# Kernel tuning notes

Hardware: AMD Instinct MI355X
Metric: run time of the kernel (lower is better)

## Reference

```python
import jax, jax.numpy as jnp
import numpy as np


def _gcn_conv(x, W, b, src, dst, n_nodes):
    """PyG-style GCNConv: XW, symmetric deg^-1/2 normalization over edges
    (with self-loops already included in src/dst), scatter-add to targets, + bias."""
    xw = x @ W  # [N, F_out]
    ones = jnp.ones(src.shape[0], dtype=xw.dtype)
    deg = jax.ops.segment_sum(ones, dst, num_segments=n_nodes)  # in-degree incl. self-loops
    dinv = jnp.where(deg > 0, jax.lax.rsqrt(jnp.maximum(deg, 1.0)), 0.0)
    norm = dinv[src] * dinv[dst]                        # [E]
    msgs = xw[src] * norm[:, None]                      # [E, F_out] gather + scale
    out = jax.ops.segment_sum(msgs, dst, num_segments=n_nodes)  # scatter-add
    return out + b


def setup_inputs() -> dict:
    key = jax.random.key(0)
    k1, k2, k3, k4 = jax.random.split(key, 4)
    N, E = 100000, 1600000
    IN, HID, OUT = 128, 64, 64
    x = jax.random.normal(k1, (N, IN), dtype=jnp.float32)
    edge_index = jax.random.randint(k2, (2, E), 0, N, dtype=jnp.int64)
    W1 = jax.random.normal(k3, (IN, HID), dtype=jnp.float32) * (1.0 / np.sqrt(IN))
    b1 = jnp.zeros((HID,), dtype=jnp.float32)
    W2 = jax.random.normal(k4, (HID, OUT), dtype=jnp.float32) * (1.0 / np.sqrt(HID))
    b2 = jnp.zeros((OUT,), dtype=jnp.float32)
    return {"x": x, "edge_index": edge_index, "W1": W1, "b1": b1, "W2": W2, "b2": b2}


def reference(x, edge_index, W1, b1, W2, b2):
    n_nodes = x.shape[0]
    # add self-loops (PyG GCNConv default add_self_loops=True)
    loops = jnp.arange(n_nodes, dtype=edge_index.dtype)
    src = jnp.concatenate([edge_index[0], loops])
    dst = jnp.concatenate([edge_index[1], loops])
    h = _gcn_conv(x, W1, b1, src, dst, n_nodes)
    h = jax.nn.relu(h)
    z = _gcn_conv(h, W2, b2, src, dst, n_nodes)
    return z
```

## Files before the change

kernel.cpp:

```cpp
#include <hip/hip_runtime.h>

#define IN_F 128
#define HID_F 64
#define BKT_SHIFT 9
#define BKT_SIZE 512
#define CHUNK 4096

typedef unsigned short ushort_t;
typedef __attribute__((ext_vector_type(8))) short bf16x8;
typedef __attribute__((ext_vector_type(8))) unsigned short u16x8;
typedef __attribute__((ext_vector_type(4))) float f32x4;

__device__ inline ushort_t f2bf(float f) {
    unsigned u = __float_as_uint(f);
    u += 0x7FFFu + ((u >> 16) & 1u);
    return (ushort_t)(u >> 16);
}
__device__ inline float bf2f(ushort_t u) {
    return __uint_as_float((unsigned)u << 16);
}


__global__ __launch_bounds__(256) void k_hist_pack(const int* __restrict__ dst,
        int* __restrict__ ghist, int E, int nbE,
        const float* __restrict__ W1, const float* __restrict__ W2,
        ushort_t* __restrict__ Bp1, ushort_t* __restrict__ Bp2) {
    int tid = threadIdx.x;
    if ((int)blockIdx.x >= nbE) {
        int id = ((int)blockIdx.x - nbE) * 256 + tid;
        int iw = (id < 8192) ? id : id - 8192;
        int j = iw & 7, lane = (iw >> 3) & 63, t = (iw >> 9) & 3, s = iw >> 11;
        int k = s * 32 + ((lane >> 4) << 3) + j;
        int n = t * 16 + (lane & 15);
        if (id < 8192)        Bp1[iw] = f2bf(W1[k * 64 + n]);
        else if (id < 12288)  Bp2[iw] = f2bf(W2[k * 64 + n]);
        return;
    }
    __shared__ int hist[256];
    hist[tid] = 0;
    __syncthreads();
    int e0 = blockIdx.x * CHUNK, e1 = min(e0 + CHUNK, E);
    for (int e = e0 + tid; e < e1; e += 256)
        atomicAdd(&hist[dst[e] >> BKT_SHIFT], 1);
    __syncthreads();
    ghist[blockIdx.x * 256 + tid] = hist[tid];
}

__global__ __launch_bounds__(256) void k_colscan(int* __restrict__ ghist,
        int* __restrict__ gcount, int nb) {
    __shared__ int s[256];
    int t = threadIdx.x;
    int b = blockIdx.x;
    int j0 = 2 * t, j1 = 2 * t + 1;
    int v0 = (j0 < nb) ? ghist[j0 * 256 + b] : 0;
    int v1 = (j1 < nb) ? ghist[j1 * 256 + b] : 0;
    int p = v0 + v1;
    s[t] = p;
    __syncthreads();
    for (int off = 1; off < 256; off <<= 1) {
        int v = (t >= off) ? s[t - off] : 0;
        __syncthreads();
        s[t] += v;
        __syncthreads();
    }
    int excl = s[t] - p;
    if (j0 < nb) ghist[j0 * 256 + b] = excl;
    if (j1 < nb) ghist[j1 * 256 + b] = excl + v0;
    if (t == 255) gcount[b] = s[255];
}

__global__ __launch_bounds__(256) void k_scatter(const int* __restrict__ src,
        const int* __restrict__ dst, const int* __restrict__ ghist,
        const int* __restrict__ gcount, unsigned* __restrict__ gbin, int E) {
    __shared__ int cur[256];
    __shared__ int s[256];
    int tid = threadIdx.x;
    int gc = gcount[tid];
    s[tid] = gc;
    __syncthreads();
    for (int off = 1; off < 256; off <<= 1) {
        int v = (tid >= off) ? s[tid - off] : 0;
        __syncthreads();
        s[tid] += v;
        __syncthreads();
    }
    cur[tid] = ghist[blockIdx.x * 256 + tid] + (s[tid] - gc);
    __syncthreads();
    int e0 = blockIdx.x * CHUNK, e1 = min(e0 + CHUNK, E);
    for (int e = e0 + tid; e < e1; e += 256) {
        int d = dst[e];
        int b = d >> BKT_SHIFT;
        int p = atomicAdd(&cur[b], 1);
        gbin[p] = ((unsigned)(d & (BKT_SIZE - 1)) << 23) | (unsigned)src[e];
    }
}

__global__ __launch_bounds__(256) void k_fill2(const unsigned* __restrict__ gbin,
        const int* __restrict__ gcount, int* __restrict__ rowptr,
        float* __restrict__ dinv, int* __restrict__ col, int N, int E) {
    __shared__ int cnt[BKT_SIZE];
    __shared__ int pos[BKT_SIZE];
    __shared__ int s[256];
    int tid = threadIdx.x;
    int b = blockIdx.x;
    int gc = gcount[tid];
    s[tid] = gc;
    __syncthreads();
    for (int off = 1; off < 256; off <<= 1) {
        int v = (tid >= off) ? s[tid - off] : 0;
        __syncthreads();
        s[tid] += v;
        __syncthreads();
    }
    int e0 = (b > 0) ? s[b - 1] : 0;
    int e1 = s[b];
    if (b == 0 && tid == 0) rowptr[N] = E;
    __syncthreads();
    cnt[tid] = 0; cnt[tid + 256] = 0;
    __syncthreads();
    for (int e = e0 + tid; e < e1; e += 256)
        atomicAdd(&cnt[gbin[e] >> 23], 1);
    __syncthreads();
    int c0 = cnt[2 * tid], c1 = cnt[2 * tid + 1];
    int p2 = c0 + c1;
    s[tid] = p2;
    __syncthreads();
    for (int off = 1; off < 256; off <<= 1) {
        int v = (tid >= off) ? s[tid - off] : 0;
        __syncthreads();
        s[tid] += v;
        __syncthreads();
    }
    int excl = s[tid] - p2;
    pos[2 * tid] = excl;
    pos[2 * tid + 1] = excl + c0;
    __syncthreads();
    int n0 = b << BKT_SHIFT;
    #pragma unroll
    for (int i = tid; i < BKT_SIZE; i += 256) {
        int n = n0 + i;
        if (n < N) {
            rowptr[n] = e0 + pos[i];
            dinv[n] = rsqrtf((float)cnt[i] + 1.0f);
        }
    }
    __syncthreads();
    for (int t = 0; t < 8; ++t) {
        for (int e = e0 + tid; e < e1; e += 256) {
            unsigned v = gbin[e];
            if (((v >> 14) & 7u) == (unsigned)t) {
                int p = atomicAdd(&pos[v >> 23], 1);
                col[e0 + p] = (int)(v & 0x7FFFFFu);
            }
        }
        __syncthreads();
    }
}

template<int K, typename AT>
__global__ __launch_bounds__(256) void k_gemm_mfma(const AT* __restrict__ A,
        const ushort_t* __restrict__ Bp, const float* __restrict__ dinv,
        ushort_t* __restrict__ out, int N) {
    int wave = threadIdx.x >> 6, lane = threadIdx.x & 63;
    int m = lane & 15, q = lane >> 4;
    int row0 = blockIdx.x * 64 + wave * 16;
    int arow = row0 + m;
    int arowc = (arow < N) ? arow : (N - 1);
    f32x4 acc[4] = {};
    #pragma unroll
    for (int s = 0; s < K / 32; ++s) {
        bf16x8 af;
        if constexpr (sizeof(AT) == 4) {
            const float* ap = (const float*)A + (size_t)arowc * K + s * 32 + q * 8;
            float4 x0 = *(const float4*)ap;
            float4 x1 = *(const float4*)(ap + 4);
            af[0] = (short)f2bf(x0.x); af[1] = (short)f2bf(x0.y);
            af[2] = (short)f2bf(x0.z); af[3] = (short)f2bf(x0.w);
            af[4] = (short)f2bf(x1.x); af[5] = (short)f2bf(x1.y);
            af[6] = (short)f2bf(x1.z); af[7] = (short)f2bf(x1.w);
        } else {
            af = *(const bf16x8*)((const ushort_t*)A + (size_t)arowc * K + s * 32 + q * 8);
        }
        #pragma unroll
        for (int t = 0; t < 4; ++t) {
            bf16x8 bf = *(const bf16x8*)(Bp + (size_t)((s * 4 + t) * 64 + lane) * 8);
            acc[t] = __builtin_amdgcn_mfma_f32_16x16x32_bf16(af, bf, acc[t], 0, 0, 0);
        }
    }
    int orow0 = row0 + q * 4;
    float4 d4 = *(const float4*)(dinv + orow0);
    #pragma unroll
    for (int r = 0; r < 4; ++r) {
        int row = orow0 + r;
        if (row < N) {
            float dn = (r == 0) ? d4.x : (r == 1) ? d4.y : (r == 2) ? d4.z : d4.w;
            #pragma unroll
            for (int t = 0; t < 4; ++t)
                out[(size_t)row * 64 + t * 16 + m] = f2bf(acc[t][r] * dn);
        }
    }
}

__global__ __launch_bounds__(256) void k_agg_gemm(const ushort_t* __restrict__ xws,
        const int* __restrict__ rowptr, const int* __restrict__ col,
        const float* __restrict__ dinv, const float* __restrict__ bias,
        const ushort_t* __restrict__ Bp2, ushort_t* __restrict__ out2, int N) {
    __shared__ ushort_t hl[32][72];
    int tid = threadIdx.x;
    int nl = tid >> 3;
    int i = tid & 7;
    int n0 = blockIdx.x * 32;
    int n = n0 + nl;
    u16x8 hz = {};
    if (n < N) {
        int beg = rowptr[n], end = rowptr[n + 1];
        float dn = dinv[n];
        const ushort_t* base = xws + i * 8;
        u16x8 sv = *(const u16x8*)(base + (size_t)n * 64);
        float a[8];
        #pragma unroll
        for (int k = 0; k < 8; ++k) a[k] = bf2f(sv[k]);
        int e = beg;
        for (; e + 8 <= end; e += 8) {
            int c[8];
            #pragma unroll
            for (int j = 0; j < 8; ++j) c[j] = col[e + j];
            u16x8 v[8];
            #pragma unroll
            for (int j = 0; j < 8; ++j) v[j] = *(const u16x8*)(base + (size_t)c[j] * 64);
            #pragma unroll
            for (int j = 0; j < 8; ++j)
                #pragma unroll
                for (int k = 0; k < 8; ++k) a[k] += bf2f(v[j][k]);
        }
        if (e + 4 <= end) {
            int c[4];
            #pragma unroll
            for (int j = 0; j < 4; ++j) c[j] = col[e + j];
            u16x8 v[4];
            #pragma unroll
            for (int j = 0; j < 4; ++j) v[j] = *(const u16x8*)(base + (size_t)c[j] * 64);
            #pragma unroll
            for (int j = 0; j < 4; ++j)
                #pragma unroll
                for (int k = 0; k < 8; ++k) a[k] += bf2f(v[j][k]);
            e += 4;
        }
        for (; e < end; ++e) {
            u16x8 v = *(const u16x8*)(base + (size_t)col[e] * 64);
            #pragma unroll
            for (int k = 0; k < 8; ++k) a[k] += bf2f(v[k]);
        }
        float4 b0 = *(const float4*)(bias + i * 8);
        float4 b1 = *(const float4*)(bias + i * 8 + 4);
        float r[8];
        r[0] = dn * a[0] + b0.x; r[1] = dn * a[1] + b0.y;
        r[2] = dn * a[2] + b0.z; r[3] = dn * a[3] + b0.w;
        r[4] = dn * a[4] + b1.x; r[5] = dn * a[5] + b1.y;
        r[6] = dn * a[6] + b1.z; r[7] = dn * a[7] + b1.w;
        #pragma unroll
        for (int k = 0; k < 8; ++k) hz[k] = f2bf(fmaxf(r[k], 0.f));
    }
    *(u16x8*)&hl[nl][i * 8] = hz;
    __syncthreads();
    int w = tid >> 6, lane = tid & 63;
    int m = lane & 15, q = lane >> 4;
    int mt = w & 1;
    int nt0 = (w >> 1) << 1;
    f32x4 acc[2] = {};
    #pragma unroll
    for (int s = 0; s < 2; ++s) {
        bf16x8 af = *(const bf16x8*)&hl[mt * 16 + m][s * 32 + q * 8];
        #pragma unroll
        for (int tt = 0; tt < 2; ++tt) {
            bf16x8 bf = *(const bf16x8*)(Bp2 + (size_t)((s * 4 + nt0 + tt) * 64 + lane) * 8);
            acc[tt] = __builtin_amdgcn_mfma_f32_16x16x32_bf16(af, bf, acc[tt], 0, 0, 0);
        }
    }
    int orow0 = n0 + mt * 16 + q * 4;
    float4 d4 = *(const float4*)(dinv + orow0);
    #pragma unroll
    for (int r = 0; r < 4; ++r) {
        int row = orow0 + r;
        if (row < N) {
            float dn = (r == 0) ? d4.x : (r == 1) ? d4.y : (r == 2) ? d4.z : d4.w;
            #pragma unroll
            for (int tt = 0; tt < 2; ++tt)
                out2[(size_t)row * 64 + (nt0 + tt) * 16 + m] = f2bf(acc[tt][r] * dn);
        }
    }
}

__global__ __launch_bounds__(256) void k_aggregate(const ushort_t* __restrict__ xws,
        const int* __restrict__ rowptr, const int* __restrict__ col,
        const float* __restrict__ dinv, const float* __restrict__ bias,
        float* __restrict__ outf, int N) {
    int n = (blockIdx.x * 256 + threadIdx.x) >> 3;
    int i = threadIdx.x & 7;
    if (n >= N) return;
    int beg = rowptr[n], end = rowptr[n + 1];
    float dn = dinv[n];
    const ushort_t* base = xws + i * 8;
    u16x8 sv = *(const u16x8*)(base + (size_t)n * 64);
    float a[8];
    #pragma unroll
    for (int k = 0; k < 8; ++k) a[k] = bf2f(sv[k]);
    int e = beg;
    for (; e + 8 <= end; e += 8) {
        int c[8];
        #pragma unroll
        for (int j = 0; j < 8; ++j) c[j] = col[e + j];
        u16x8 v[8];
        #pragma unroll
        for (int j = 0; j < 8; ++j) v[j] = *(const u16x8*)(base + (size_t)c[j] * 64);
        #pragma unroll
        for (int j = 0; j < 8; ++j)
            #pragma unroll
            for (int k = 0; k < 8; ++k) a[k] += bf2f(v[j][k]);
    }
    if (e + 4 <= end) {
        int c[4];
        #pragma unroll
        for (int j = 0; j < 4; ++j) c[j] = col[e + j];
        u16x8 v[4];
        #pragma unroll
        for (int j = 0; j < 4; ++j) v[j] = *(const u16x8*)(base + (size_t)c[j] * 64);
        #pragma unroll
        for (int j = 0; j < 4; ++j)
            #pragma unroll
            for (int k = 0; k < 8; ++k) a[k] += bf2f(v[j][k]);
        e += 4;
    }
    for (; e < end; ++e) {
        u16x8 v = *(const u16x8*)(base + (size_t)col[e] * 64);
        #pragma unroll
        for (int k = 0; k < 8; ++k) a[k] += bf2f(v[k]);
    }
    float4 b0 = *(const float4*)(bias + i * 8);
    float4 b1 = *(const float4*)(bias + i * 8 + 4);
    float4 o0 = {dn * a[0] + b0.x, dn * a[1] + b0.y, dn * a[2] + b0.z, dn * a[3] + b0.w};
    float4 o1 = {dn * a[4] + b1.x, dn * a[5] + b1.y, dn * a[6] + b1.z, dn * a[7] + b1.w};
    *(float4*)(outf + (size_t)n * 64 + i * 8) = o0;
    *(float4*)(outf + (size_t)n * 64 + i * 8 + 4) = o1;
}


extern "C" void kernel_launch(void* const* d_in, const int* in_sizes, int n_in,
                              void* d_out, int out_size, void* d_ws, size_t ws_size,
                              hipStream_t stream) {
    const float* x  = (const float*)d_in[0];
    const int*   ei = (const int*)d_in[1];
    const float* W1 = (const float*)d_in[2];
    const float* b1 = (const float*)d_in[3];
    const float* W2 = (const float*)d_in[4];
    const float* b2 = (const float*)d_in[5];
    float* out = (float*)d_out;

    const int N = in_sizes[0] / IN_F;
    const int E = in_sizes[1] / 2;
    const int* src = ei;
    const int* dst = ei + E;

    char* ws = (char*)d_ws;
    const size_t MB = 1u << 20;
    int*      gcount  = (int*)     (ws + 12288);
    ushort_t* Bp1     = (ushort_t*)(ws + 16384);
    ushort_t* Bp2     = (ushort_t*)(ws + 49152);
    int*      rowptr  = (int*)     (ws + 1 * MB);
    float*    dinv    = (float*)   (ws + 2 * MB);
    unsigned* gbin    = (unsigned*)(ws + 3 * MB);
    int*      ghist   = (int*)     (ws + 10 * MB);
    int*      col     = (int*)     (ws + 11 * MB);
    ushort_t* xws     = (ushort_t*)(ws + 20 * MB);
    ushort_t* xws2    = (ushort_t*)(ws + 36 * MB);

    const int nbE = (E + CHUNK - 1) / CHUNK;
    const int nbB = (N + BKT_SIZE - 1) / BKT_SIZE;
    const int nbG = (N + 63) / 64;
    const int nbA = (N * 8 + 255) / 256;

    k_hist_pack<<<nbE + 48, 256, 0, stream>>>(dst, ghist, E, nbE, W1, W2, Bp1, Bp2);
    k_colscan<<<256, 256, 0, stream>>>(ghist, gcount, nbE);
    k_scatter<<<nbE, 256, 0, stream>>>(src, dst, ghist, gcount, gbin, E);
    k_fill2  <<<nbB, 256, 0, stream>>>(gbin, gcount, rowptr, dinv, col, N, E);

    k_gemm_mfma<IN_F, float><<<nbG, 256, 0, stream>>>(x, Bp1, dinv, xws, N);
    k_agg_gemm<<<nbA, 256, 0, stream>>>(xws, rowptr, col, dinv, b1, Bp2, xws2, N);
    k_aggregate<<<nbA, 256, 0, stream>>>(xws2, rowptr, col, dinv, b2, out, N);
}
```

Baseline: 261.8 us.

## Bin edges by dst bucket and src sub-range in radix scatter, drop 8-pass fill

The coarse histogram and scatter now key on the destination bucket combined with 3 bits of the source index (2048 bins instead of 256). Within each bucket, gbin entries are therefore already grouped by source sub-range, so the fill kernel can place column indices in a single pass. The old fill rescanned the bucket 8 times with a sync after each pass to get source-locality ordering. The trade-off is a histogram 8x larger (more ghist traffic, more colscan blocks, larger shared arrays) and an extra src read in the histogram kernel.

```diff
diff --git a/kernel.cpp b/kernel.cpp
--- a/kernel.cpp
+++ b/kernel.cpp
@@ -4,6 +4,7 @@
 #define HID_F 64
 #define BKT_SHIFT 9
 #define BKT_SIZE 512
+#define NH 2048
 #define CHUNK 4096
 
 typedef unsigned short ushort_t;
@@ -22,7 +23,7 @@
 
 
 __global__ __launch_bounds__(256) void k_hist_pack(const int* __restrict__ dst,
-        int* __restrict__ ghist, int E, int nbE,
+        const int* __restrict__ src, int* __restrict__ ghist, int E, int nbE,
         const float* __restrict__ W1, const float* __restrict__ W2,
         ushort_t* __restrict__ Bp1, ushort_t* __restrict__ Bp2) {
     int tid = threadIdx.x;
@@ -36,14 +37,19 @@
         else if (id < 12288)  Bp2[iw] = f2bf(W2[k * 64 + n]);
         return;
     }
-    __shared__ int hist[256];
-    hist[tid] = 0;
+    __shared__ int hist[NH];
+    #pragma unroll
+    for (int k = 0; k < 8; ++k) hist[tid + k * 256] = 0;
     __syncthreads();
     int e0 = blockIdx.x * CHUNK, e1 = min(e0 + CHUNK, E);
-    for (int e = e0 + tid; e < e1; e += 256)
-        atomicAdd(&hist[dst[e] >> BKT_SHIFT], 1);
-    __syncthreads();
-    ghist[blockIdx.x * 256 + tid] = hist[tid];
+    for (int e = e0 + tid; e < e1; e += 256) {
+        int d = dst[e], sc = src[e];
+        atomicAdd(&hist[((d >> BKT_SHIFT) << 3) | ((sc >> 14) & 7)], 1);
+    }
+    __syncthreads();
+    #pragma unroll
+    for (int k = 0; k < 8; ++k)
+        ghist[(size_t)blockIdx.x * NH + tid + k * 256] = hist[tid + k * 256];
 }
 
 __global__ __launch_bounds__(256) void k_colscan(int* __restrict__ ghist,
@@ -52,8 +58,8 @@
     int t = threadIdx.x;
     int b = blockIdx.x;
     int j0 = 2 * t, j1 = 2 * t + 1;
-    int v0 = (j0 < nb) ? ghist[j0 * 256 + b] : 0;
-    int v1 = (j1 < nb) ? ghist[j1 * 256 + b] : 0;
+    int v0 = (j0 < nb) ? ghist[(size_t)j0 * NH + b] : 0;
+    int v1 = (j1 < nb) ? ghist[(size_t)j1 * NH + b] : 0;
     int p = v0 + v1;
     s[t] = p;
     __syncthreads();
@@ -64,19 +70,21 @@
         __syncthreads();
     }
     int excl = s[t] - p;
-    if (j0 < nb) ghist[j0 * 256 + b] = excl;
-    if (j1 < nb) ghist[j1 * 256 + b] = excl + v0;
+    if (j0 < nb) ghist[(size_t)j0 * NH + b] = excl;
+    if (j1 < nb) ghist[(size_t)j1 * NH + b] = excl + v0;
     if (t == 255) gcount[b] = s[255];
 }
 
 __global__ __launch_bounds__(256) void k_scatter(const int* __restrict__ src,
         const int* __restrict__ dst, const int* __restrict__ ghist,
         const int* __restrict__ gcount, unsigned* __restrict__ gbin, int E) {
-    __shared__ int cur[256];
+    __shared__ int cur[NH];
     __shared__ int s[256];
     int tid = threadIdx.x;
-    int gc = gcount[tid];
-    s[tid] = gc;
+    int g[8]; int lsum = 0;
+    #pragma unroll
+    for (int k = 0; k < 8; ++k) { g[k] = gcount[tid * 8 + k]; lsum += g[k]; }
+    s[tid] = lsum;
     __syncthreads();
     for (int off = 1; off < 256; off <<= 1) {
         int v = (tid >= off) ? s[tid - off] : 0;
@@ -84,27 +92,35 @@
         s[tid] += v;
         __syncthreads();
     }
-    cur[tid] = ghist[blockIdx.x * 256 + tid] + (s[tid] - gc);
+    int run = s[tid] - lsum;
+    #pragma unroll
+    for (int k = 0; k < 8; ++k) {
+        cur[tid * 8 + k] = run + ghist[(size_t)blockIdx.x * NH + tid * 8 + k];
+        run += g[k];
+    }
     __syncthreads();
     int e0 = blockIdx.x * CHUNK, e1 = min(e0 + CHUNK, E);
     for (int e = e0 + tid; e < e1; e += 256) {
-        int d = dst[e];
-        int b = d >> BKT_SHIFT;
-        int p = atomicAdd(&cur[b], 1);
-        gbin[p] = ((unsigned)(d & (BKT_SIZE - 1)) << 23) | (unsigned)src[e];
+        int d = dst[e], sc = src[e];
+        int key = ((d >> BKT_SHIFT) << 3) | ((sc >> 14) & 7);
+        int p = atomicAdd(&cur[key], 1);
+        gbin[p] = ((unsigned)(d & (BKT_SIZE - 1)) << 23) | (unsigned)sc;
     }
 }
 
 __global__ __launch_bounds__(256) void k_fill2(const unsigned* __restrict__ gbin,
         const int* __restrict__ gcount, int* __restrict__ rowptr,
         float* __restrict__ dinv, int* __restrict__ col, int N, int E) {
+    __shared__ int base[NH];
     __shared__ int cnt[BKT_SIZE];
     __shared__ int pos[BKT_SIZE];
     __shared__ int s[256];
     int tid = threadIdx.x;
     int b = blockIdx.x;
-    int gc = gcount[tid];
-    s[tid] = gc;
+    int g[8]; int lsum = 0;
+    #pragma unroll
+    for (int k = 0; k < 8; ++k) { g[k] = gcount[tid * 8 + k]; lsum += g[k]; }
+    s[tid] = lsum;
     __syncthreads();
     for (int off = 1; off < 256; off <<= 1) {
         int v = (tid >= off) ? s[tid - off] : 0;
@@ -112,8 +128,12 @@
         s[tid] += v;
         __syncthreads();
     }
-    int e0 = (b > 0) ? s[b - 1] : 0;
-    int e1 = s[b];
+    int run = s[tid] - lsum;
+    #pragma unroll
+    for (int k = 0; k < 8; ++k) { base[tid * 8 + k] = run; run += g[k]; }
+    __syncthreads();
+    int e0 = base[b * 8];
+    int e1 = (b * 8 + 8 < NH) ? base[b * 8 + 8] : E;
     if (b == 0 && tid == 0) rowptr[N] = E;
     __syncthreads();
     cnt[tid] = 0; cnt[tid + 256] = 0;
@@ -145,15 +165,10 @@
         }
     }
     __syncthreads();
-    for (int t = 0; t < 8; ++t) {
-        for (int e = e0 + tid; e < e1; e += 256) {
-            unsigned v = gbin[e];
-            if (((v >> 14) & 7u) == (unsigned)t) {
-                int p = atomicAdd(&pos[v >> 23], 1);
-                col[e0 + p] = (int)(v & 0x7FFFFFu);
-            }
-        }
-        __syncthreads();
+    for (int e = e0 + tid; e < e1; e += 256) {
+        unsigned v = gbin[e];
+        int p = atomicAdd(&pos[v >> 23], 1);
+        col[e0 + p] = (int)(v & 0x7FFFFFu);
     }
 }
 
@@ -363,24 +378,24 @@
 
     char* ws = (char*)d_ws;
     const size_t MB = 1u << 20;
-    int*      gcount  = (int*)     (ws + 12288);
+    int*      gcount  = (int*)     (ws + 4096);
     ushort_t* Bp1     = (ushort_t*)(ws + 16384);
     ushort_t* Bp2     = (ushort_t*)(ws + 49152);
     int*      rowptr  = (int*)     (ws + 1 * MB);
     float*    dinv    = (float*)   (ws + 2 * MB);
     unsigned* gbin    = (unsigned*)(ws + 3 * MB);
-    int*      ghist   = (int*)     (ws + 10 * MB);
     int*      col     = (int*)     (ws + 11 * MB);
     ushort_t* xws     = (ushort_t*)(ws + 20 * MB);
     ushort_t* xws2    = (ushort_t*)(ws + 36 * MB);
+    int*      ghist   = (int*)     (ws + 52 * MB);
 
     const int nbE = (E + CHUNK - 1) / CHUNK;
     const int nbB = (N + BKT_SIZE - 1) / BKT_SIZE;
     const int nbG = (N + 63) / 64;
     const int nbA = (N * 8 + 255) / 256;
 
-    k_hist_pack<<<nbE + 48, 256, 0, stream>>>(dst, ghist, E, nbE, W1, W2, Bp1, Bp2);
-    k_colscan<<<256, 256, 0, stream>>>(ghist, gcount, nbE);
+    k_hist_pack<<<nbE + 48, 256, 0, stream>>>(dst, src, ghist, E, nbE, W1, W2, Bp1, Bp2);
+    k_colscan<<<NH, 256, 0, stream>>>(ghist, gcount, nbE);
     k_scatter<<<nbE, 256, 0, stream>>>(src, dst, ghist, gcount, gbin, E);
     k_fill2  <<<nbB, 256, 0, stream>>>(gbin, gcount, rowptr, dinv, col, N, E);
 
```

Measured after the change: 243.8 us. 1.07x faster.
